# Kernel tuning notes

Hardware: AMD Instinct MI355X
Metric: run time of the kernel (lower is better)

Reference implementation:

```python
import jax, jax.numpy as jnp
import numpy as np

DIM = 768
HEADS = 12
HEAD_DIM = DIM // HEADS
B, S = 2, 2048
EPS = 1e-5


def _layernorm(x, w, b):
    mu = jnp.mean(x, axis=-1, keepdims=True)
    var = jnp.mean(jnp.square(x - mu), axis=-1, keepdims=True)
    return (x - mu) * jax.lax.rsqrt(var + EPS) * w + b


def setup_inputs() -> dict:
    key = jax.random.key(0)
    ks = jax.random.split(key, 16)
    sc = 1.0 / np.sqrt(DIM)
    inp = {
        'x': jax.random.normal(ks[0], (B, S, DIM), jnp.float32),
        'bias': jax.random.normal(ks[1], (HEADS, B, S, S), jnp.float32),
        'mask': jax.random.randint(ks[2], (1, B, S, S), 0, 2, jnp.int32),
        'ln1_w': jnp.ones((DIM,), jnp.float32),
        'ln1_b': jnp.zeros((DIM,), jnp.float32),
        'wq': jax.random.normal(ks[3], (DIM, DIM), jnp.float32) * sc,
        'bq': jnp.zeros((DIM,), jnp.float32),
        'wk': jax.random.normal(ks[4], (DIM, DIM), jnp.float32) * sc,
        'bk': jnp.zeros((DIM,), jnp.float32),
        'wv': jax.random.normal(ks[5], (DIM, DIM), jnp.float32) * sc,
        'bv': jnp.zeros((DIM,), jnp.float32),
        'wo': jax.random.normal(ks[6], (DIM, DIM), jnp.float32) * sc,
        'bo': jnp.zeros((DIM,), jnp.float32),
        'ln2_w': jnp.ones((DIM,), jnp.float32),
        'ln2_b': jnp.zeros((DIM,), jnp.float32),
        'w1': jax.random.normal(ks[7], (DIM, DIM), jnp.float32) * sc,
        'b1': jnp.zeros((DIM,), jnp.float32),
        'w2': jax.random.normal(ks[8], (DIM, DIM), jnp.float32) * sc,
        'b2': jnp.zeros((DIM,), jnp.float32),
    }
    return inp


def _split_heads(t):
    # [B,S,D] -> [H,B,S,Dh]  (matches torch view + permute(2,0,1,3))
    return t.reshape(B, S, HEADS, HEAD_DIM).transpose(2, 0, 1, 3)


def reference(x, bias, mask, ln1_w, ln1_b, wq, bq, wk, bk, wv, bv, wo, bo,
              ln2_w, ln2_b, w1, b1, w2, b2):
    xn = _layernorm(x, ln1_w, ln1_b)
    q = _split_heads(xn @ wq + bq)
    k = _split_heads(xn @ wk + bk)
    v = _split_heads(xn @ wv + bv)
    # scores: [H,B,Sq,Sk]; bias added BEFORE scaling, then masked, then scaled softmax
    scores = jnp.einsum('hbqd,hbkd->hbqk', q, k) + bias
    scores = jnp.where(mask == 0, jnp.float32(-1e20), scores)
    probs = jax.nn.softmax(scores / np.sqrt(HEAD_DIM), axis=-1)
    attn = jnp.einsum('hbqk,hbkd->hbqd', probs, v)
    attn = attn.transpose(1, 2, 0, 3).reshape(B, S, DIM)
    x = x + (attn @ wo + bo)
    xn = _layernorm(x, ln2_w, ln2_b)
    h = jax.nn.relu(xn @ w1 + b1)
    x = x + (h @ w2 + b2)
    return x
```

## Files before the change

### kernel.cpp

```cpp
#include <hip/hip_runtime.h>
#include <math.h>

#define DIMM 768
#define SEQ 2048
#define BATB 2
#define NHEAD 12
#define DHEAD 64
#define ROWS 4096

typedef __attribute__((ext_vector_type(8))) short bf16x8;
typedef __attribute__((ext_vector_type(4))) float f32x4;
typedef unsigned short ushort_t;
typedef unsigned int uint_t;

union U16 { int4 i; ushort_t u[8]; };

__device__ __forceinline__ ushort_t f2b(float f) {
    uint_t u = __float_as_uint(f);
    return (ushort_t)((u + 0x7FFFu + ((u >> 16) & 1u)) >> 16);
}

__device__ __forceinline__ void gl16(const ushort_t* g, ushort_t* l) {
    __builtin_amdgcn_global_load_lds(
        (const __attribute__((address_space(1))) unsigned int*)g,
        (__attribute__((address_space(3))) unsigned int*)l,
        16, 0, 0);
}

struct WPtrs { const float* s[6]; };
struct BPtrs { const float* p[3]; };

__global__ __launch_bounds__(256) void wtrans_k(WPtrs wp, ushort_t* __restrict__ dst)
{
    __shared__ float T[64][65];
    int wi = blockIdx.z;
    const float* in = wp.s[wi];
    ushort_t* out = dst + (size_t)wi * (DIMM * DIMM);
    int kb = blockIdx.y * 64, nb = blockIdx.x * 64;
    int t = threadIdx.x;
    int kl = t >> 4, nl = (t & 15) * 4;
    #pragma unroll
    for (int it = 0; it < 4; it++) {
        float4 a = *(const float4*)&in[(size_t)(kb + kl + it * 16) * DIMM + nb + nl];
        T[kl + it * 16][nl + 0] = a.x;
        T[kl + it * 16][nl + 1] = a.y;
        T[kl + it * 16][nl + 2] = a.z;
        T[kl + it * 16][nl + 3] = a.w;
    }
    __syncthreads();
    int no = t >> 2, ko = (t & 3) * 16;
    #pragma unroll
    for (int j = 0; j < 2; j++) {
        U16 u;
        #pragma unroll
        for (int c = 0; c < 8; c++) u.u[c] = f2b(T[ko + j * 8 + c][no]);
        *(int4*)&out[(size_t)(nb + no) * DIMM + kb + ko + j * 8] = u.i;
    }
}

__global__ __launch_bounds__(256) void ln_k(const float* __restrict__ x,
                                            const float* __restrict__ w,
                                            const float* __restrict__ b,
                                            ushort_t* __restrict__ out)
{
    int row = blockIdx.x;
    int tid = threadIdx.x;
    const float* xr = x + (size_t)row * DIMM;
    float v0 = xr[tid], v1 = xr[tid + 256], v2 = xr[tid + 512];
    float s  = v0 + v1 + v2;
    float ss = v0 * v0 + v1 * v1 + v2 * v2;
    #pragma unroll
    for (int off = 32; off > 0; off >>= 1) {
        s  += __shfl_down(s,  off);
        ss += __shfl_down(ss, off);
    }
    __shared__ float ws_[4], wss_[4];
    __shared__ float mu_s, rs_s;
    int lane = tid & 63, wid = tid >> 6;
    if (lane == 0) { ws_[wid] = s; wss_[wid] = ss; }
    __syncthreads();
    if (tid == 0) {
        float S1 = ws_[0] + ws_[1] + ws_[2] + ws_[3];
        float S2 = wss_[0] + wss_[1] + wss_[2] + wss_[3];
        float m = S1 * (1.0f / DIMM);
        float var = S2 * (1.0f / DIMM) - m * m;
        mu_s = m;
        rs_s = rsqrtf(var + 1e-5f);
    }
    __syncthreads();
    float mu = mu_s, rs = rs_s;
    ushort_t* orow = out + (size_t)row * DIMM;
    orow[tid]       = f2b((v0 - mu) * rs * w[tid]       + b[tid]);
    orow[tid + 256] = f2b((v1 - mu) * rs * w[tid + 256] + b[tid + 256]);
    orow[tid + 512] = f2b((v2 - mu) * rs * w[tid + 512] + b[tid + 512]);
}

template<int ASRC, int OMODE, bool RELU, bool RES, int NB>
__global__ __launch_bounds__(256) void mgemm_k(const ushort_t* __restrict__ A,
                                               const ushort_t* __restrict__ BT,
                                               BPtrs bias,
                                               const float* __restrict__ res,
                                               void* __restrict__ outv)
{
    __shared__ alignas(16) ushort_t Asl[8 * 64 * 8];
    __shared__ alignas(16) ushort_t Bsl[8 * 64 * 8];
    int tid = threadIdx.x;
    int lane = tid & 63, w = tid >> 6;
    int colBase = blockIdx.x * 64, rowBase = blockIdx.y * 64;

    size_t offA[2], offB[2];
    ushort_t* dstA[2];
    ushort_t* dstB[2];
    const size_t strideA = (ASRC == 1) ? (size_t)64 : (size_t)BATB * SEQ * DHEAD;
    #pragma unroll
    for (int i = 0; i < 2; i++) {
        int slot = i * 4 + w;
        {
            int sm = ((slot >> 1) << 4) | (lane & 15);
            int c  = ((slot & 1) << 2) | (lane >> 4);
            if (ASRC == 1) {
                offA[i] = (size_t)(rowBase + sm) * DIMM + 8 * c;
            } else {
                int r = rowBase + sm;
                offA[i] = ((size_t)(r >> 11) * SEQ + (r & 2047)) * DHEAD + 8 * c;
            }
            dstA[i] = &Asl[(size_t)(i * 256 + w * 64) * 8];
        }
        {
            int sm = ((slot & 3) << 4) | (lane & 15);
            int c  = ((slot >> 2) << 2) | (lane >> 4);
            offB[i] = (size_t)(colBase + sm) * DIMM + 8 * c;
            dstB[i] = &Bsl[(size_t)(i * 256 + w * 64) * 8];
        }
    }

    f32x4 acc[4];
    #pragma unroll
    for (int nt = 0; nt < 4; nt++) { f32x4 z = {0.f, 0.f, 0.f, 0.f}; acc[nt] = z; }

    for (int t = 0; t < DIMM / 64; t++) {
        gl16(A  + offA[0], dstA[0]);
        gl16(A  + offA[1], dstA[1]);
        gl16(BT + offB[0], dstB[0]);
        gl16(BT + offB[1], dstB[1]);
        offA[0] += strideA; offA[1] += strideA;
        offB[0] += 64;      offB[1] += 64;
        __syncthreads();
        bf16x8 a0 = *(bf16x8*)&Asl[((w * 2 + 0) * 64 + lane) * 8];
        bf16x8 a1 = *(bf16x8*)&Asl[((w * 2 + 1) * 64 + lane) * 8];
        #pragma unroll
        for (int nt = 0; nt < 4; nt++) {
            bf16x8 b0 = *(bf16x8*)&Bsl[((0 * 4 + nt) * 64 + lane) * 8];
            bf16x8 b1 = *(bf16x8*)&Bsl[((1 * 4 + nt) * 64 + lane) * 8];
            acc[nt] = __builtin_amdgcn_mfma_f32_16x16x32_bf16(a0, b0, acc[nt], 0, 0, 0);
            acc[nt] = __builtin_amdgcn_mfma_f32_16x16x32_bf16(a1, b1, acc[nt], 0, 0, 0);
        }
        __syncthreads();
    }
    int wi = (NB == 3) ? (int)(blockIdx.x / 12) : 0;
    const float* bp_ = bias.p[wi];
    int nLoc0 = colBase - wi * DIMM;
    int col_l = lane & 15, quad = lane >> 4;
    #pragma unroll
    for (int nt = 0; nt < 4; nt++) {
        int n = colBase + nt * 16 + col_l;
        float bn = bp_[nLoc0 + nt * 16 + col_l];
        #pragma unroll
        for (int r = 0; r < 4; r++) {
            int row = rowBase + w * 16 + quad * 4 + r;
            float v = acc[nt][r] + bn;
            if (RELU) v = fmaxf(v, 0.0f);
            if (RES)  v += res[(size_t)row * DIMM + n];
            if (OMODE == 0) {
                ((float*)outv)[(size_t)row * DIMM + n] = v;
            } else if (OMODE == 1) {
                ((ushort_t*)outv)[(size_t)row * DIMM + n] = f2b(v);
            } else {
                ((ushort_t*)outv)[((size_t)((n >> 6) * BATB + (row >> 11)) * SEQ + (row & 2047)) * DHEAD + (n & 63)] = f2b(v);
            }
        }
    }
}

__global__ __launch_bounds__(256) void attn_k(const ushort_t* __restrict__ q,
                                              const ushort_t* __restrict__ k,
                                              const ushort_t* __restrict__ v,
                                              const float* __restrict__ bias,
                                              const int* __restrict__ mask,
                                              ushort_t* __restrict__ out)
{
    __shared__ alignas(16) ushort_t Kf[8 * 64 * 8];
    __shared__ alignas(16) ushort_t Vf[8 * 64 * 8];
    __shared__ alignas(16) ushort_t Pf[8 * 64 * 8];
    int tid = threadIdx.x, lane = tid & 63, w = tid >> 6;
    int col_l = lane & 15, quad = lane >> 4;
    int qbase = blockIdx.x * 64;
    int hb = blockIdx.y;
    const ushort_t* qp = q + (size_t)hb * SEQ * DHEAD;
    const ushort_t* kp = k + (size_t)hb * SEQ * DHEAD;
    const ushort_t* vp = v + (size_t)hb * SEQ * DHEAD;
    const float* bp = bias + (size_t)hb * SEQ * SEQ;
    const int*   mp = mask + (size_t)(hb & 1) * SEQ * SEQ;

    bf16x8 qF0 = *(const bf16x8*)&qp[(size_t)(qbase + w * 16 + col_l) * DHEAD + (quad * 8)];
    bf16x8 qF1 = *(const bf16x8*)&qp[(size_t)(qbase + w * 16 + col_l) * DHEAD + 32 + (quad * 8)];

    size_t offK[2];
    ushort_t* dstK[2];
    #pragma unroll
    for (int i = 0; i < 2; i++) {
        int slot = i * 4 + w;
        int sn = ((slot & 3) << 4) | (lane & 15);
        int c  = ((slot >> 2) << 2) | (lane >> 4);
        offK[i] = (size_t)sn * DHEAD + 8 * c;
        dstK[i] = &Kf[(size_t)(i * 256 + w * 64) * 8];
    }

    f32x4 O[4];
    #pragma unroll
    for (int nt = 0; nt < 4; nt++) { f32x4 z = {0.f, 0.f, 0.f, 0.f}; O[nt] = z; }
    float m_run[4], l_run[4];
    #pragma unroll
    for (int r = 0; r < 4; r++) { m_run[r] = -1e30f; l_run[r] = 0.0f; }

    int j0 = (tid >> 3) * 2, e0 = (tid & 7) * 8;
    const float C2 = 0.18033688011112042f;

    for (int kvb = 0; kvb < SEQ; kvb += 64) {
        gl16(kp + (size_t)kvb * DHEAD + offK[0], dstK[0]);
        gl16(kp + (size_t)kvb * DHEAD + offK[1], dstK[1]);
        {
            U16 g0, g1;
            g0.i = *(const int4*)&vp[(size_t)(kvb + j0) * DHEAD + e0];
            g1.i = *(const int4*)&vp[(size_t)(kvb + j0 + 1) * DHEAD + e0];
            int js = j0 >> 5, grp = (j0 & 31) >> 3, i0 = j0 & 7;
            #pragma unroll
            for (int c = 0; c < 8; c++) {
                int n = e0 + c;
                uint_t pk = (uint_t)g0.u[c] | ((uint_t)g1.u[c] << 16);
                int idx = ((js * 4 + (n >> 4)) * 64 + ((n & 15) | (grp << 4))) * 8 + i0;
                *(uint_t*)&Vf[idx] = pk;
            }
        }
        float bl[4][4]; int ml[4][4];
        #pragma unroll
        for (int nt = 0; nt < 4; nt++) {
            int col = kvb + nt * 16 + col_l;
            #pragma unroll
            for (int r = 0; r < 4; r++) {
                int qrow = qbase + w * 16 + quad * 4 + r;
                bl[nt][r] = bp[(size_t)qrow * SEQ + col];
                ml[nt][r] = mp[(size_t)qrow * SEQ + col];
            }
        }
        __syncthreads();
        f32x4 S[4];
        #pragma unroll
        for (int nt = 0; nt < 4; nt++) {
            bf16x8 b0 = *(bf16x8*)&Kf[((0 * 4 + nt) * 64 + lane) * 8];
            bf16x8 b1 = *(bf16x8*)&Kf[((1 * 4 + nt) * 64 + lane) * 8];
            f32x4 z = {0.f, 0.f, 0.f, 0.f};
            z = __builtin_amdgcn_mfma_f32_16x16x32_bf16(qF0, b0, z, 0, 0, 0);
            S[nt] = __builtin_amdgcn_mfma_f32_16x16x32_bf16(qF1, b1, z, 0, 0, 0);
        }
        float lg[4][4];
        #pragma unroll
        for (int nt = 0; nt < 4; nt++)
            #pragma unroll
            for (int r = 0; r < 4; r++)
                lg[nt][r] = ml[nt][r] ? (S[nt][r] + bl[nt][r]) * C2 : -2.0e18f;
        #pragma unroll
        for (int r = 0; r < 4; r++) {
            float mx = fmaxf(fmaxf(lg[0][r], lg[1][r]), fmaxf(lg[2][r], lg[3][r]));
            mx = fmaxf(mx, __shfl_xor(mx, 1));
            mx = fmaxf(mx, __shfl_xor(mx, 2));
            mx = fmaxf(mx, __shfl_xor(mx, 4));
            mx = fmaxf(mx, __shfl_xor(mx, 8));
            if (!__all(mx - m_run[r] <= 4.0f)) {
                float mnew = fmaxf(m_run[r], mx);
                float alpha = __builtin_amdgcn_exp2f(m_run[r] - mnew);
                m_run[r] = mnew;
                l_run[r] *= alpha;
                #pragma unroll
                for (int nt = 0; nt < 4; nt++) O[nt][r] *= alpha;
            }
            float mcur = m_run[r];
            float rs = 0.0f;
            #pragma unroll
            for (int nt = 0; nt < 4; nt++) {
                float p = __builtin_amdgcn_exp2f(lg[nt][r] - mcur);
                lg[nt][r] = p;
                rs += p;
            }
            rs += __shfl_xor(rs, 1);
            rs += __shfl_xor(rs, 2);
            rs += __shfl_xor(rs, 4);
            rs += __shfl_xor(rs, 8);
            l_run[r] += rs;
        }
        #pragma unroll
        for (int nt = 0; nt < 4; nt++) {
            int j = nt * 16 + col_l;
            #pragma unroll
            for (int r = 0; r < 4; r++) {
                ushort_t pu = f2b(lg[nt][r]);
                uint_t po = (uint_t)(unsigned)__shfl_xor((int)pu, 1);
                if ((lane & 1) == 0) {
                    int m = quad * 4 + r;
                    int idx = ((w * 2 + (j >> 5)) * 64 + (m | (((j & 31) >> 3) << 4))) * 8 + (j & 7);
                    *(uint_t*)&Pf[idx] = (uint_t)pu | (po << 16);
                }
            }
        }
        #pragma unroll
        for (int js = 0; js < 2; js++) {
            bf16x8 pF = *(bf16x8*)&Pf[((w * 2 + js) * 64 + lane) * 8];
            #pragma unroll
            for (int nt = 0; nt < 4; nt++) {
                bf16x8 vF = *(bf16x8*)&Vf[((js * 4 + nt) * 64 + lane) * 8];
                O[nt] = __builtin_amdgcn_mfma_f32_16x16x32_bf16(pF, vF, O[nt], 0, 0, 0);
            }
        }
        __syncthreads();
    }
    float inv[4];
    #pragma unroll
    for (int r = 0; r < 4; r++) inv[r] = 1.0f / l_run[r];
    #pragma unroll
    for (int nt = 0; nt < 4; nt++)
        #pragma unroll
        for (int r = 0; r < 4; r++) {
            int row = qbase + w * 16 + quad * 4 + r;
            out[((size_t)hb * SEQ + row) * DHEAD + nt * 16 + col_l] = f2b(O[nt][r] * inv[r]);
        }
}

extern "C" void kernel_launch(void* const* d_in, const int* in_sizes, int n_in,
                              void* d_out, int out_size, void* d_ws, size_t ws_size,
                              hipStream_t stream)
{
    const float* x    = (const float*)d_in[0];
    const float* bias = (const float*)d_in[1];
    const int*   mask = (const int*)d_in[2];
    const float* ln1w = (const float*)d_in[3];
    const float* ln1b = (const float*)d_in[4];
    const float* wq   = (const float*)d_in[5];
    const float* bq   = (const float*)d_in[6];
    const float* wk   = (const float*)d_in[7];
    const float* bk   = (const float*)d_in[8];
    const float* wv   = (const float*)d_in[9];
    const float* bv   = (const float*)d_in[10];
    const float* wo   = (const float*)d_in[11];
    const float* bo   = (const float*)d_in[12];
    const float* ln2w = (const float*)d_in[13];
    const float* ln2b = (const float*)d_in[14];
    const float* w1   = (const float*)d_in[15];
    const float* b1   = (const float*)d_in[16];
    const float* w2   = (const float*)d_in[17];
    const float* b2   = (const float*)d_in[18];

    const size_t WSZ = (size_t)DIMM * DIMM;
    const size_t ABUF = (size_t)ROWS * DIMM;

    ushort_t* wsu  = (ushort_t*)d_ws;
    ushort_t* wT   = wsu;
    ushort_t* qb   = wsu + 6 * WSZ;
    ushort_t* kbuf = qb + ABUF;
    ushort_t* vbuf = kbuf + ABUF;
    ushort_t* xn1  = vbuf + ABUF;
    float*    x1   = (float*)(xn1 + ABUF);
    ushort_t* hid  = qb;

    WPtrs wp; wp.s[0] = wq; wp.s[1] = wk; wp.s[2] = wv; wp.s[3] = wo; wp.s[4] = w1; wp.s[5] = w2;
    BPtrs bqkv; bqkv.p[0] = bq; bqkv.p[1] = bk; bqkv.p[2] = bv;
    BPtrs bbo;  bbo.p[0]  = bo; bbo.p[1]  = bo; bbo.p[2]  = bo;
    BPtrs bb1;  bb1.p[0]  = b1; bb1.p[1]  = b1; bb1.p[2]  = b1;
    BPtrs bb2;  bb2.p[0]  = b2; bb2.p[1]  = b2; bb2.p[2]  = b2;

    dim3 gg(12, 64), gb(256);
    wtrans_k<<<dim3(12, 12, 6), 256, 0, stream>>>(wp, wT);
    ln_k<<<ROWS, 256, 0, stream>>>(x, ln1w, ln1b, xn1);
    mgemm_k<1, 2, false, false, 3><<<dim3(36, 64), gb, 0, stream>>>(xn1, wT, bqkv, nullptr, qb);
    attn_k<<<dim3(32, 24), 256, 0, stream>>>(qb, kbuf, vbuf, bias, mask, xn1);
    mgemm_k<2, 0, false, true, 1><<<gg, gb, 0, stream>>>(xn1, wT + 3 * WSZ, bbo, x, x1);
    ln_k<<<ROWS, 256, 0, stream>>>(x1, ln2w, ln2b, xn1);
    mgemm_k<1, 1, true, false, 1><<<gg, gb, 0, stream>>>(xn1, wT + 4 * WSZ, bb1, nullptr, hid);
    mgemm_k<1, 0, false, true, 1><<<gg, gb, 0, stream>>>(hid, wT + 5 * WSZ, bb2, x1, (float*)d_out);
}
```

Measured before the change: 783.0 us.

## Double-buffer LDS tiles in GEMM and attention kernels with register prefetch

```diff
diff --git a/kernel.cpp b/kernel.cpp
--- a/kernel.cpp
+++ b/kernel.cpp
@@ -102,15 +102,14 @@
                                                const float* __restrict__ res,
                                                void* __restrict__ outv)
 {
-    __shared__ alignas(16) ushort_t Asl[8 * 64 * 8];
-    __shared__ alignas(16) ushort_t Bsl[8 * 64 * 8];
+    __shared__ alignas(16) ushort_t Asl[2][8 * 64 * 8];
+    __shared__ alignas(16) ushort_t Bsl[2][8 * 64 * 8];
     int tid = threadIdx.x;
     int lane = tid & 63, w = tid >> 6;
     int colBase = blockIdx.x * 64, rowBase = blockIdx.y * 64;
 
     size_t offA[2], offB[2];
-    ushort_t* dstA[2];
-    ushort_t* dstB[2];
+    int lbA[2], lbB[2];
     const size_t strideA = (ASRC == 1) ? (size_t)64 : (size_t)BATB * SEQ * DHEAD;
     #pragma unroll
     for (int i = 0; i < 2; i++) {
@@ -124,13 +123,13 @@
                 int r = rowBase + sm;
                 offA[i] = ((size_t)(r >> 11) * SEQ + (r & 2047)) * DHEAD + 8 * c;
             }
-            dstA[i] = &Asl[(size_t)(i * 256 + w * 64) * 8];
+            lbA[i] = (i * 256 + w * 64) * 8;
         }
         {
             int sm = ((slot & 3) << 4) | (lane & 15);
             int c  = ((slot >> 2) << 2) | (lane >> 4);
             offB[i] = (size_t)(colBase + sm) * DIMM + 8 * c;
-            dstB[i] = &Bsl[(size_t)(i * 256 + w * 64) * 8];
+            lbB[i] = (i * 256 + w * 64) * 8;
         }
     }
 
@@ -138,24 +137,51 @@
     #pragma unroll
     for (int nt = 0; nt < 4; nt++) { f32x4 z = {0.f, 0.f, 0.f, 0.f}; acc[nt] = z; }
 
-    for (int t = 0; t < DIMM / 64; t++) {
-        gl16(A  + offA[0], dstA[0]);
-        gl16(A  + offA[1], dstA[1]);
-        gl16(BT + offB[0], dstB[0]);
-        gl16(BT + offB[1], dstB[1]);
+    const int NT = DIMM / 64;
+
+    gl16(A  + offA[0], &Asl[0][lbA[0]]);
+    gl16(A  + offA[1], &Asl[0][lbA[1]]);
+    gl16(BT + offB[0], &Bsl[0][lbB[0]]);
+    gl16(BT + offB[1], &Bsl[0][lbB[1]]);
+    offA[0] += strideA; offA[1] += strideA;
+    offB[0] += 64;      offB[1] += 64;
+
+    int p = 0;
+    for (int t = 0; t < NT - 1; ++t) {
+        gl16(A  + offA[0], &Asl[p ^ 1][lbA[0]]);
+        gl16(A  + offA[1], &Asl[p ^ 1][lbA[1]]);
+        gl16(BT + offB[0], &Bsl[p ^ 1][lbB[0]]);
+        gl16(BT + offB[1], &Bsl[p ^ 1][lbB[1]]);
         offA[0] += strideA; offA[1] += strideA;
         offB[0] += 64;      offB[1] += 64;
-        __syncthreads();
-        bf16x8 a0 = *(bf16x8*)&Asl[((w * 2 + 0) * 64 + lane) * 8];
-        bf16x8 a1 = *(bf16x8*)&Asl[((w * 2 + 1) * 64 + lane) * 8];
+        asm volatile("s_waitcnt vmcnt(4)" ::: "memory");
+        __builtin_amdgcn_sched_barrier(0);
+        __builtin_amdgcn_s_barrier();
+        bf16x8 a0 = *(bf16x8*)&Asl[p][((w * 2 + 0) * 64 + lane) * 8];
+        bf16x8 a1 = *(bf16x8*)&Asl[p][((w * 2 + 1) * 64 + lane) * 8];
         #pragma unroll
         for (int nt = 0; nt < 4; nt++) {
-            bf16x8 b0 = *(bf16x8*)&Bsl[((0 * 4 + nt) * 64 + lane) * 8];
-            bf16x8 b1 = *(bf16x8*)&Bsl[((1 * 4 + nt) * 64 + lane) * 8];
+            bf16x8 b0 = *(bf16x8*)&Bsl[p][((0 * 4 + nt) * 64 + lane) * 8];
+            bf16x8 b1 = *(bf16x8*)&Bsl[p][((1 * 4 + nt) * 64 + lane) * 8];
             acc[nt] = __builtin_amdgcn_mfma_f32_16x16x32_bf16(a0, b0, acc[nt], 0, 0, 0);
             acc[nt] = __builtin_amdgcn_mfma_f32_16x16x32_bf16(a1, b1, acc[nt], 0, 0, 0);
         }
-        __syncthreads();
+        __builtin_amdgcn_s_barrier();
+        p ^= 1;
+    }
+    asm volatile("s_waitcnt vmcnt(0)" ::: "memory");
+    __builtin_amdgcn_sched_barrier(0);
+    __builtin_amdgcn_s_barrier();
+    {
+        bf16x8 a0 = *(bf16x8*)&Asl[p][((w * 2 + 0) * 64 + lane) * 8];
+        bf16x8 a1 = *(bf16x8*)&Asl[p][((w * 2 + 1) * 64 + lane) * 8];
+        #pragma unroll
+        for (int nt = 0; nt < 4; nt++) {
+            bf16x8 b0 = *(bf16x8*)&Bsl[p][((0 * 4 + nt) * 64 + lane) * 8];
+            bf16x8 b1 = *(bf16x8*)&Bsl[p][((1 * 4 + nt) * 64 + lane) * 8];
+            acc[nt] = __builtin_amdgcn_mfma_f32_16x16x32_bf16(a0, b0, acc[nt], 0, 0, 0);
+            acc[nt] = __builtin_amdgcn_mfma_f32_16x16x32_bf16(a1, b1, acc[nt], 0, 0, 0);
+        }
     }
     int wi = (NB == 3) ? (int)(blockIdx.x / 12) : 0;
     const float* bp_ = bias.p[wi];
@@ -189,8 +215,8 @@
                                               const int* __restrict__ mask,
                                               ushort_t* __restrict__ out)
 {
-    __shared__ alignas(16) ushort_t Kf[8 * 64 * 8];
-    __shared__ alignas(16) ushort_t Vf[8 * 64 * 8];
+    __shared__ alignas(16) ushort_t Kf[2][8 * 64 * 8];
+    __shared__ alignas(16) ushort_t Vf[2][8 * 64 * 8];
     __shared__ alignas(16) ushort_t Pf[8 * 64 * 8];
     int tid = threadIdx.x, lane = tid & 63, w = tid >> 6;
     int col_l = lane & 15, quad = lane >> 4;
@@ -205,16 +231,19 @@
     bf16x8 qF0 = *(const bf16x8*)&qp[(size_t)(qbase + w * 16 + col_l) * DHEAD + (quad * 8)];
     bf16x8 qF1 = *(const bf16x8*)&qp[(size_t)(qbase + w * 16 + col_l) * DHEAD + 32 + (quad * 8)];
 
-    size_t offK[2];
-    ushort_t* dstK[2];
-    #pragma unroll
-    for (int i = 0; i < 2; i++) {
-        int slot = i * 4 + w;
-        int sn = ((slot & 3) << 4) | (lane & 15);
-        int c  = ((slot >> 2) << 2) | (lane >> 4);
-        offK[i] = (size_t)sn * DHEAD + 8 * c;
-        dstK[i] = &Kf[(size_t)(i * 256 + w * 64) * 8];
-    }
+    int sn = tid >> 2, sko = (tid & 3) * 16;
+    int kidx[2];
+    #pragma unroll
+    for (int jj = 0; jj < 2; jj++) {
+        int kk = sko + jj * 8;
+        int slot = (kk >> 5) * 4 + (sn >> 4);
+        int ln = (sn & 15) | (((kk & 31) >> 3) << 4);
+        kidx[jj] = (slot * 64 + ln) * 8;
+    }
+    size_t koff = (size_t)sn * DHEAD + sko;
+    int j0 = (tid >> 3) * 2, e0 = (tid & 7) * 8;
+    int js = j0 >> 5, grp = (j0 & 31) >> 3, i0 = j0 & 7;
+    size_t voff = (size_t)j0 * DHEAD + e0;
 
     f32x4 O[4];
     #pragma unroll
@@ -223,25 +252,35 @@
     #pragma unroll
     for (int r = 0; r < 4; r++) { m_run[r] = -1e30f; l_run[r] = 0.0f; }
 
-    int j0 = (tid >> 3) * 2, e0 = (tid & 7) * 8;
     const float C2 = 0.18033688011112042f;
 
+    int4 kr0 = *(const int4*)&kp[koff];
+    int4 kr1 = *(const int4*)&kp[koff + 8];
+    int4 vr0 = *(const int4*)&vp[voff];
+    int4 vr1 = *(const int4*)&vp[voff + DHEAD];
+    *(int4*)&Kf[0][kidx[0]] = kr0;
+    *(int4*)&Kf[0][kidx[1]] = kr1;
+    {
+        U16 g0, g1; g0.i = vr0; g1.i = vr1;
+        #pragma unroll
+        for (int c = 0; c < 8; c++) {
+            int n = e0 + c;
+            uint_t pk = (uint_t)g0.u[c] | ((uint_t)g1.u[c] << 16);
+            int idx = ((js * 4 + (n >> 4)) * 64 + ((n & 15) | (grp << 4))) * 8 + i0;
+            *(uint_t*)&Vf[0][idx] = pk;
+        }
+    }
+    {
+        size_t b1 = (size_t)64 * DHEAD;
+        kr0 = *(const int4*)&kp[b1 + koff];
+        kr1 = *(const int4*)&kp[b1 + koff + 8];
+        vr0 = *(const int4*)&vp[b1 + voff];
+        vr1 = *(const int4*)&vp[b1 + voff + DHEAD];
+    }
+    __syncthreads();
+
+    int p = 0;
     for (int kvb = 0; kvb < SEQ; kvb += 64) {
-        gl16(kp + (size_t)kvb * DHEAD + offK[0], dstK[0]);
-        gl16(kp + (size_t)kvb * DHEAD + offK[1], dstK[1]);
-        {
-            U16 g0, g1;
-            g0.i = *(const int4*)&vp[(size_t)(kvb + j0) * DHEAD + e0];
-            g1.i = *(const int4*)&vp[(size_t)(kvb + j0 + 1) * DHEAD + e0];
-            int js = j0 >> 5, grp = (j0 & 31) >> 3, i0 = j0 & 7;
-            #pragma unroll
-            for (int c = 0; c < 8; c++) {
-                int n = e0 + c;
-                uint_t pk = (uint_t)g0.u[c] | ((uint_t)g1.u[c] << 16);
-                int idx = ((js * 4 + (n >> 4)) * 64 + ((n & 15) | (grp << 4))) * 8 + i0;
-                *(uint_t*)&Vf[idx] = pk;
-            }
-        }
         float bl[4][4]; int ml[4][4];
         #pragma unroll
         for (int nt = 0; nt < 4; nt++) {
@@ -253,16 +292,17 @@
                 ml[nt][r] = mp[(size_t)qrow * SEQ + col];
             }
         }
-        __syncthreads();
         f32x4 S[4];
+        __builtin_amdgcn_s_setprio(1);
         #pragma unroll
         for (int nt = 0; nt < 4; nt++) {
-            bf16x8 b0 = *(bf16x8*)&Kf[((0 * 4 + nt) * 64 + lane) * 8];
-            bf16x8 b1 = *(bf16x8*)&Kf[((1 * 4 + nt) * 64 + lane) * 8];
+            bf16x8 b0 = *(bf16x8*)&Kf[p][((0 * 4 + nt) * 64 + lane) * 8];
+            bf16x8 b1 = *(bf16x8*)&Kf[p][((1 * 4 + nt) * 64 + lane) * 8];
             f32x4 z = {0.f, 0.f, 0.f, 0.f};
             z = __builtin_amdgcn_mfma_f32_16x16x32_bf16(qF0, b0, z, 0, 0, 0);
             S[nt] = __builtin_amdgcn_mfma_f32_16x16x32_bf16(qF1, b1, z, 0, 0, 0);
         }
+        __builtin_amdgcn_s_setprio(0);
         float lg[4][4];
         #pragma unroll
         for (int nt = 0; nt < 4; nt++)
@@ -288,15 +328,36 @@
             float rs = 0.0f;
             #pragma unroll
             for (int nt = 0; nt < 4; nt++) {
-                float p = __builtin_amdgcn_exp2f(lg[nt][r] - mcur);
-                lg[nt][r] = p;
-                rs += p;
+                float pp = __builtin_amdgcn_exp2f(lg[nt][r] - mcur);
+                lg[nt][r] = pp;
+                rs += pp;
             }
             rs += __shfl_xor(rs, 1);
             rs += __shfl_xor(rs, 2);
             rs += __shfl_xor(rs, 4);
             rs += __shfl_xor(rs, 8);
             l_run[r] += rs;
+        }
+        if (kvb + 64 < SEQ) {
+            *(int4*)&Kf[p ^ 1][kidx[0]] = kr0;
+            *(int4*)&Kf[p ^ 1][kidx[1]] = kr1;
+            {
+                U16 g0, g1; g0.i = vr0; g1.i = vr1;
+                #pragma unroll
+                for (int c = 0; c < 8; c++) {
+                    int n = e0 + c;
+                    uint_t pk = (uint_t)g0.u[c] | ((uint_t)g1.u[c] << 16);
+                    int idx = ((js * 4 + (n >> 4)) * 64 + ((n & 15) | (grp << 4))) * 8 + i0;
+                    *(uint_t*)&Vf[p ^ 1][idx] = pk;
+                }
+            }
+            if (kvb + 128 < SEQ) {
+                size_t b2 = (size_t)(kvb + 128) * DHEAD;
+                kr0 = *(const int4*)&kp[b2 + koff];
+                kr1 = *(const int4*)&kp[b2 + koff + 8];
+                vr0 = *(const int4*)&vp[b2 + voff];
+                vr1 = *(const int4*)&vp[b2 + voff + DHEAD];
+            }
         }
         #pragma unroll
         for (int nt = 0; nt < 4; nt++) {
@@ -312,16 +373,19 @@
                 }
             }
         }
-        #pragma unroll
-        for (int js = 0; js < 2; js++) {
-            bf16x8 pF = *(bf16x8*)&Pf[((w * 2 + js) * 64 + lane) * 8];
+        __builtin_amdgcn_s_setprio(1);
+        #pragma unroll
+        for (int jss = 0; jss < 2; jss++) {
+            bf16x8 pF = *(bf16x8*)&Pf[((w * 2 + jss) * 64 + lane) * 8];
             #pragma unroll
             for (int nt = 0; nt < 4; nt++) {
-                bf16x8 vF = *(bf16x8*)&Vf[((js * 4 + nt) * 64 + lane) * 8];
+                bf16x8 vF = *(bf16x8*)&Vf[p][((jss * 4 + nt) * 64 + lane) * 8];
                 O[nt] = __builtin_amdgcn_mfma_f32_16x16x32_bf16(pF, vF, O[nt], 0, 0, 0);
             }
         }
+        __builtin_amdgcn_s_setprio(0);
         __syncthreads();
+        p ^= 1;
     }
     float inv[4];
     #pragma unroll
```

Measured after the change: 835.2 us. 6.7% more time.

## Double-buffer K/V tiles and prefetch bias/mask in attention loop

Applied to the files above, without the earlier changes.

```diff
diff --git a/kernel.cpp b/kernel.cpp
--- a/kernel.cpp
+++ b/kernel.cpp
@@ -182,15 +182,15 @@
     }
 }
 
-__global__ __launch_bounds__(256) void attn_k(const ushort_t* __restrict__ q,
-                                              const ushort_t* __restrict__ k,
-                                              const ushort_t* __restrict__ v,
-                                              const float* __restrict__ bias,
-                                              const int* __restrict__ mask,
-                                              ushort_t* __restrict__ out)
+__global__ __launch_bounds__(256, 4) void attn_k(const ushort_t* __restrict__ q,
+                                                 const ushort_t* __restrict__ k,
+                                                 const ushort_t* __restrict__ v,
+                                                 const float* __restrict__ bias,
+                                                 const int* __restrict__ mask,
+                                                 ushort_t* __restrict__ out)
 {
-    __shared__ alignas(16) ushort_t Kf[8 * 64 * 8];
-    __shared__ alignas(16) ushort_t Vf[8 * 64 * 8];
+    __shared__ alignas(16) ushort_t Kf[2][8 * 64 * 8];
+    __shared__ alignas(16) ushort_t Vf[2][8 * 64 * 8];
     __shared__ alignas(16) ushort_t Pf[8 * 64 * 8];
     int tid = threadIdx.x, lane = tid & 63, w = tid >> 6;
     int col_l = lane & 15, quad = lane >> 4;
@@ -205,16 +205,18 @@
     bf16x8 qF0 = *(const bf16x8*)&qp[(size_t)(qbase + w * 16 + col_l) * DHEAD + (quad * 8)];
     bf16x8 qF1 = *(const bf16x8*)&qp[(size_t)(qbase + w * 16 + col_l) * DHEAD + 32 + (quad * 8)];
 
-    size_t offK[2];
-    ushort_t* dstK[2];
+    size_t offK[2]; int lbK[2];
     #pragma unroll
     for (int i = 0; i < 2; i++) {
         int slot = i * 4 + w;
         int sn = ((slot & 3) << 4) | (lane & 15);
         int c  = ((slot >> 2) << 2) | (lane >> 4);
         offK[i] = (size_t)sn * DHEAD + 8 * c;
-        dstK[i] = &Kf[(size_t)(i * 256 + w * 64) * 8];
-    }
+        lbK[i] = (i * 256 + w * 64) * 8;
+    }
+    int j0 = (tid >> 3) * 2, e0 = (tid & 7) * 8;
+    int js = j0 >> 5, grp = (j0 & 31) >> 3, i0 = j0 & 7;
+    size_t voff = (size_t)j0 * DHEAD + e0;
 
     f32x4 O[4];
     #pragma unroll
@@ -223,52 +225,88 @@
     #pragma unroll
     for (int r = 0; r < 4; r++) { m_run[r] = -1e30f; l_run[r] = 0.0f; }
 
-    int j0 = (tid >> 3) * 2, e0 = (tid & 7) * 8;
     const float C2 = 0.18033688011112042f;
 
+    gl16(kp + offK[0], &Kf[0][lbK[0]]);
+    gl16(kp + offK[1], &Kf[0][lbK[1]]);
+    int4 vr0 = *(const int4*)&vp[voff];
+    int4 vr1 = *(const int4*)&vp[voff + DHEAD];
+    float blN[4][4]; int mlN[4][4];
+    #pragma unroll
+    for (int nt = 0; nt < 4; nt++) {
+        int col = nt * 16 + col_l;
+        #pragma unroll
+        for (int r = 0; r < 4; r++) {
+            int qrow = qbase + w * 16 + quad * 4 + r;
+            blN[nt][r] = bp[(size_t)qrow * SEQ + col];
+            mlN[nt][r] = mp[(size_t)qrow * SEQ + col];
+        }
+    }
+    {
+        U16 g0, g1; g0.i = vr0; g1.i = vr1;
+        #pragma unroll
+        for (int c = 0; c < 8; c++) {
+            int n = e0 + c;
+            uint_t pk = (uint_t)g0.u[c] | ((uint_t)g1.u[c] << 16);
+            int idx = ((js * 4 + (n >> 4)) * 64 + ((n & 15) | (grp << 4))) * 8 + i0;
+            *(uint_t*)&Vf[0][idx] = pk;
+        }
+    }
+    {
+        size_t b1 = (size_t)64 * DHEAD;
+        vr0 = *(const int4*)&vp[b1 + voff];
+        vr1 = *(const int4*)&vp[b1 + voff + DHEAD];
+    }
+    __syncthreads();
+
+    int p = 0;
     for (int kvb = 0; kvb < SEQ; kvb += 64) {
-        gl16(kp + (size_t)kvb * DHEAD + offK[0], dstK[0]);
-        gl16(kp + (size_t)kvb * DHEAD + offK[1], dstK[1]);
-        {
-            U16 g0, g1;
-            g0.i = *(const int4*)&vp[(size_t)(kvb + j0) * DHEAD + e0];
-            g1.i = *(const int4*)&vp[(size_t)(kvb + j0 + 1) * DHEAD + e0];
-            int js = j0 >> 5, grp = (j0 & 31) >> 3, i0 = j0 & 7;
-            #pragma unroll
-            for (int c = 0; c < 8; c++) {
-                int n = e0 + c;
-                uint_t pk = (uint_t)g0.u[c] | ((uint_t)g1.u[c] << 16);
-                int idx = ((js * 4 + (n >> 4)) * 64 + ((n & 15) | (grp << 4))) * 8 + i0;
-                *(uint_t*)&Vf[idx] = pk;
-            }
-        }
-        float bl[4][4]; int ml[4][4];
+        f32x4 S[4];
+        __builtin_amdgcn_s_setprio(1);
         #pragma unroll
         for (int nt = 0; nt < 4; nt++) {
-            int col = kvb + nt * 16 + col_l;
-            #pragma unroll
-            for (int r = 0; r < 4; r++) {
-                int qrow = qbase + w * 16 + quad * 4 + r;
-                bl[nt][r] = bp[(size_t)qrow * SEQ + col];
-                ml[nt][r] = mp[(size_t)qrow * SEQ + col];
-            }
-        }
-        __syncthreads();
-        f32x4 S[4];
-        #pragma unroll
-        for (int nt = 0; nt < 4; nt++) {
-            bf16x8 b0 = *(bf16x8*)&Kf[((0 * 4 + nt) * 64 + lane) * 8];
-            bf16x8 b1 = *(bf16x8*)&Kf[((1 * 4 + nt) * 64 + lane) * 8];
+            bf16x8 b0 = *(bf16x8*)&Kf[p][((0 * 4 + nt) * 64 + lane) * 8];
+            bf16x8 b1 = *(bf16x8*)&Kf[p][((1 * 4 + nt) * 64 + lane) * 8];
             f32x4 z = {0.f, 0.f, 0.f, 0.f};
             z = __builtin_amdgcn_mfma_f32_16x16x32_bf16(qF0, b0, z, 0, 0, 0);
             S[nt] = __builtin_amdgcn_mfma_f32_16x16x32_bf16(qF1, b1, z, 0, 0, 0);
         }
+        __builtin_amdgcn_s_setprio(0);
         float lg[4][4];
         #pragma unroll
         for (int nt = 0; nt < 4; nt++)
             #pragma unroll
             for (int r = 0; r < 4; r++)
-                lg[nt][r] = ml[nt][r] ? (S[nt][r] + bl[nt][r]) * C2 : -2.0e18f;
+                lg[nt][r] = mlN[nt][r] ? (S[nt][r] + blN[nt][r]) * C2 : -2.0e18f;
+        if (kvb + 64 < SEQ) {
+            #pragma unroll
+            for (int nt = 0; nt < 4; nt++) {
+                int col = kvb + 64 + nt * 16 + col_l;
+                #pragma unroll
+                for (int r = 0; r < 4; r++) {
+                    int qrow = qbase + w * 16 + quad * 4 + r;
+                    blN[nt][r] = bp[(size_t)qrow * SEQ + col];
+                    mlN[nt][r] = mp[(size_t)qrow * SEQ + col];
+                }
+            }
+            gl16(kp + (size_t)(kvb + 64) * DHEAD + offK[0], &Kf[p ^ 1][lbK[0]]);
+            gl16(kp + (size_t)(kvb + 64) * DHEAD + offK[1], &Kf[p ^ 1][lbK[1]]);
+            {
+                U16 g0, g1; g0.i = vr0; g1.i = vr1;
+                #pragma unroll
+                for (int c = 0; c < 8; c++) {
+                    int n = e0 + c;
+                    uint_t pk = (uint_t)g0.u[c] | ((uint_t)g1.u[c] << 16);
+                    int idx = ((js * 4 + (n >> 4)) * 64 + ((n & 15) | (grp << 4))) * 8 + i0;
+                    *(uint_t*)&Vf[p ^ 1][idx] = pk;
+                }
+            }
+            if (kvb + 128 < SEQ) {
+                size_t b2 = (size_t)(kvb + 128) * DHEAD;
+                vr0 = *(const int4*)&vp[b2 + voff];
+                vr1 = *(const int4*)&vp[b2 + voff + DHEAD];
+            }
+        }
         #pragma unroll
         for (int r = 0; r < 4; r++) {
             float mx = fmaxf(fmaxf(lg[0][r], lg[1][r]), fmaxf(lg[2][r], lg[3][r]));
@@ -288,9 +326,9 @@
             float rs = 0.0f;
             #pragma unroll
             for (int nt = 0; nt < 4; nt++) {
-                float p = __builtin_amdgcn_exp2f(lg[nt][r] - mcur);
-                lg[nt][r] = p;
-                rs += p;
+                float pp = __builtin_amdgcn_exp2f(lg[nt][r] - mcur);
+                lg[nt][r] = pp;
+                rs += pp;
             }
             rs += __shfl_xor(rs, 1);
             rs += __shfl_xor(rs, 2);
@@ -312,16 +350,19 @@
                 }
             }
         }
-        #pragma unroll
-        for (int js = 0; js < 2; js++) {
-            bf16x8 pF = *(bf16x8*)&Pf[((w * 2 + js) * 64 + lane) * 8];
+        __builtin_amdgcn_s_setprio(1);
+        #pragma unroll
+        for (int jss = 0; jss < 2; jss++) {
+            bf16x8 pF = *(bf16x8*)&Pf[((w * 2 + jss) * 64 + lane) * 8];
             #pragma unroll
             for (int nt = 0; nt < 4; nt++) {
-                bf16x8 vF = *(bf16x8*)&Vf[((js * 4 + nt) * 64 + lane) * 8];
+                bf16x8 vF = *(bf16x8*)&Vf[p][((jss * 4 + nt) * 64 + lane) * 8];
                 O[nt] = __builtin_amdgcn_mfma_f32_16x16x32_bf16(pF, vF, O[nt], 0, 0, 0);
             }
         }
+        __builtin_amdgcn_s_setprio(0);
         __syncthreads();
+        p ^= 1;
     }
     float inv[4];
     #pragma unroll
```

Measured after the change: 1.381 ms. 1.76x slower.

## Enlarge GEMM block tile to 128x128 with 2x2 warp layout and register reuse

Applied to the files above, without the earlier changes.

```diff
diff --git a/kernel.cpp b/kernel.cpp
--- a/kernel.cpp
+++ b/kernel.cpp
@@ -102,81 +102,86 @@
                                                const float* __restrict__ res,
                                                void* __restrict__ outv)
 {
-    __shared__ alignas(16) ushort_t Asl[8 * 64 * 8];
-    __shared__ alignas(16) ushort_t Bsl[8 * 64 * 8];
+    __shared__ alignas(16) ushort_t Asl[16 * 64 * 8];
+    __shared__ alignas(16) ushort_t Bsl[16 * 64 * 8];
     int tid = threadIdx.x;
     int lane = tid & 63, w = tid >> 6;
-    int colBase = blockIdx.x * 64, rowBase = blockIdx.y * 64;
-
-    size_t offA[2], offB[2];
-    ushort_t* dstA[2];
-    ushort_t* dstB[2];
+    int wr = w >> 1, wc = w & 1;
+    int colBase = blockIdx.x * 128, rowBase = blockIdx.y * 128;
+
+    size_t offA[4], offB[4];
+    ushort_t* dstA[4];
+    ushort_t* dstB[4];
     const size_t strideA = (ASRC == 1) ? (size_t)64 : (size_t)BATB * SEQ * DHEAD;
     #pragma unroll
-    for (int i = 0; i < 2; i++) {
-        int slot = i * 4 + w;
-        {
-            int sm = ((slot >> 1) << 4) | (lane & 15);
-            int c  = ((slot & 1) << 2) | (lane >> 4);
-            if (ASRC == 1) {
-                offA[i] = (size_t)(rowBase + sm) * DIMM + 8 * c;
-            } else {
-                int r = rowBase + sm;
-                offA[i] = ((size_t)(r >> 11) * SEQ + (r & 2047)) * DHEAD + 8 * c;
-            }
-            dstA[i] = &Asl[(size_t)(i * 256 + w * 64) * 8];
-        }
-        {
-            int sm = ((slot & 3) << 4) | (lane & 15);
-            int c  = ((slot >> 2) << 2) | (lane >> 4);
-            offB[i] = (size_t)(colBase + sm) * DIMM + 8 * c;
-            dstB[i] = &Bsl[(size_t)(i * 256 + w * 64) * 8];
-        }
-    }
-
-    f32x4 acc[4];
-    #pragma unroll
-    for (int nt = 0; nt < 4; nt++) { f32x4 z = {0.f, 0.f, 0.f, 0.f}; acc[nt] = z; }
+    for (int i = 0; i < 4; i++) {
+        int s  = i * 4 + w;
+        int mt = s >> 1, ks = s & 1;
+        int rr = mt * 16 + (lane & 15);
+        int kk = ks * 32 + (lane >> 4) * 8;
+        if (ASRC == 1) {
+            offA[i] = (size_t)(rowBase + rr) * DIMM + kk;
+        } else {
+            int r = rowBase + rr;
+            offA[i] = ((size_t)(r >> 11) * SEQ + (r & 2047)) * DHEAD + kk;
+        }
+        dstA[i] = &Asl[(size_t)s * 64 * 8];
+        offB[i] = (size_t)(colBase + rr) * DIMM + kk;
+        dstB[i] = &Bsl[(size_t)s * 64 * 8];
+    }
+
+    f32x4 acc[4][4];
+    #pragma unroll
+    for (int mi = 0; mi < 4; mi++)
+        #pragma unroll
+        for (int ni = 0; ni < 4; ni++) { f32x4 z = {0.f, 0.f, 0.f, 0.f}; acc[mi][ni] = z; }
 
     for (int t = 0; t < DIMM / 64; t++) {
-        gl16(A  + offA[0], dstA[0]);
-        gl16(A  + offA[1], dstA[1]);
-        gl16(BT + offB[0], dstB[0]);
-        gl16(BT + offB[1], dstB[1]);
-        offA[0] += strideA; offA[1] += strideA;
-        offB[0] += 64;      offB[1] += 64;
+        #pragma unroll
+        for (int i = 0; i < 4; i++) { gl16(A  + offA[i], dstA[i]); offA[i] += strideA; }
+        #pragma unroll
+        for (int i = 0; i < 4; i++) { gl16(BT + offB[i], dstB[i]); offB[i] += 64; }
         __syncthreads();
-        bf16x8 a0 = *(bf16x8*)&Asl[((w * 2 + 0) * 64 + lane) * 8];
-        bf16x8 a1 = *(bf16x8*)&Asl[((w * 2 + 1) * 64 + lane) * 8];
-        #pragma unroll
-        for (int nt = 0; nt < 4; nt++) {
-            bf16x8 b0 = *(bf16x8*)&Bsl[((0 * 4 + nt) * 64 + lane) * 8];
-            bf16x8 b1 = *(bf16x8*)&Bsl[((1 * 4 + nt) * 64 + lane) * 8];
-            acc[nt] = __builtin_amdgcn_mfma_f32_16x16x32_bf16(a0, b0, acc[nt], 0, 0, 0);
-            acc[nt] = __builtin_amdgcn_mfma_f32_16x16x32_bf16(a1, b1, acc[nt], 0, 0, 0);
+        bf16x8 b[4][2];
+        #pragma unroll
+        for (int ni = 0; ni < 4; ni++)
+            #pragma unroll
+            for (int ks = 0; ks < 2; ks++)
+                b[ni][ks] = *(bf16x8*)&Bsl[((((wc * 4 + ni) * 2 + ks)) * 64 + lane) * 8];
+        #pragma unroll
+        for (int mi = 0; mi < 4; mi++) {
+            bf16x8 a0 = *(bf16x8*)&Asl[((((wr * 4 + mi) * 2 + 0)) * 64 + lane) * 8];
+            bf16x8 a1 = *(bf16x8*)&Asl[((((wr * 4 + mi) * 2 + 1)) * 64 + lane) * 8];
+            #pragma unroll
+            for (int ni = 0; ni < 4; ni++) {
+                acc[mi][ni] = __builtin_amdgcn_mfma_f32_16x16x32_bf16(a0, b[ni][0], acc[mi][ni], 0, 0, 0);
+                acc[mi][ni] = __builtin_amdgcn_mfma_f32_16x16x32_bf16(a1, b[ni][1], acc[mi][ni], 0, 0, 0);
+            }
         }
         __syncthreads();
     }
-    int wi = (NB == 3) ? (int)(blockIdx.x / 12) : 0;
+    int wi = (NB == 3) ? (colBase / DIMM) : 0;
     const float* bp_ = bias.p[wi];
-    int nLoc0 = colBase - wi * DIMM;
     int col_l = lane & 15, quad = lane >> 4;
     #pragma unroll
-    for (int nt = 0; nt < 4; nt++) {
-        int n = colBase + nt * 16 + col_l;
-        float bn = bp_[nLoc0 + nt * 16 + col_l];
-        #pragma unroll
-        for (int r = 0; r < 4; r++) {
-            int row = rowBase + w * 16 + quad * 4 + r;
-            float v = acc[nt][r] + bn;
-            if (RELU) v = fmaxf(v, 0.0f);
-            if (RES)  v += res[(size_t)row * DIMM + n];
-            if (OMODE == 0) {
-                ((float*)outv)[(size_t)row * DIMM + n] = v;
-            } else if (OMODE == 1) {
-                ((ushort_t*)outv)[(size_t)row * DIMM + n] = f2b(v);
-            } else {
-                ((ushort_t*)outv)[((size_t)((n >> 6) * BATB + (row >> 11)) * SEQ + (row & 2047)) * DHEAD + (n & 63)] = f2b(v);
+    for (int ni = 0; ni < 4; ni++) {
+        int n = colBase + wc * 64 + ni * 16 + col_l;
+        float bn = bp_[n - wi * DIMM];
+        #pragma unroll
+        for (int mi = 0; mi < 4; mi++) {
+            #pragma unroll
+            for (int r = 0; r < 4; r++) {
+                int row = rowBase + wr * 64 + mi * 16 + quad * 4 + r;
+                float v = acc[mi][ni][r] + bn;
+                if (RELU) v = fmaxf(v, 0.0f);
+                if (RES)  v += res[(size_t)row * DIMM + n];
+                if (OMODE == 0) {
+                    ((float*)outv)[(size_t)row * DIMM + n] = v;
+                } else if (OMODE == 1) {
+                    ((ushort_t*)outv)[(size_t)row * DIMM + n] = f2b(v);
+                } else {
+                    ((ushort_t*)outv)[((size_t)((n >> 6) * BATB + (row >> 11)) * SEQ + (row & 2047)) * DHEAD + (n & 63)] = f2b(v);
+                }
             }
         }
     }
@@ -288,9 +293,9 @@
             float rs = 0.0f;
             #pragma unroll
             for (int nt = 0; nt < 4; nt++) {
-                float p = __builtin_amdgcn_exp2f(lg[nt][r] - mcur);
-                lg[nt][r] = p;
-                rs += p;
+                float pp = __builtin_amdgcn_exp2f(lg[nt][r] - mcur);
+                lg[nt][r] = pp;
+                rs += pp;
             }
             rs += __shfl_xor(rs, 1);
             rs += __shfl_xor(rs, 2);
@@ -313,11 +318,11 @@
             }
         }
         #pragma unroll
-        for (int js = 0; js < 2; js++) {
-            bf16x8 pF = *(bf16x8*)&Pf[((w * 2 + js) * 64 + lane) * 8];
+        for (int jss = 0; jss < 2; jss++) {
+            bf16x8 pF = *(bf16x8*)&Pf[((w * 2 + jss) * 64 + lane) * 8];
             #pragma unroll
             for (int nt = 0; nt < 4; nt++) {
-                bf16x8 vF = *(bf16x8*)&Vf[((js * 4 + nt) * 64 + lane) * 8];
+                bf16x8 vF = *(bf16x8*)&Vf[((jss * 4 + nt) * 64 + lane) * 8];
                 O[nt] = __builtin_amdgcn_mfma_f32_16x16x32_bf16(pF, vF, O[nt], 0, 0, 0);
             }
         }
@@ -377,10 +382,10 @@
     BPtrs bb1;  bb1.p[0]  = b1; bb1.p[1]  = b1; bb1.p[2]  = b1;
     BPtrs bb2;  bb2.p[0]  = b2; bb2.p[1]  = b2; bb2.p[2]  = b2;
 
-    dim3 gg(12, 64), gb(256);
+    dim3 gg(6, 32), gb(256);
     wtrans_k<<<dim3(12, 12, 6), 256, 0, stream>>>(wp, wT);
     ln_k<<<ROWS, 256, 0, stream>>>(x, ln1w, ln1b, xn1);
-    mgemm_k<1, 2, false, false, 3><<<dim3(36, 64), gb, 0, stream>>>(xn1, wT, bqkv, nullptr, qb);
+    mgemm_k<1, 2, false, false, 3><<<dim3(18, 32), gb, 0, stream>>>(xn1, wT, bqkv, nullptr, qb);
     attn_k<<<dim3(32, 24), 256, 0, stream>>>(qb, kbuf, vbuf, bias, mask, xn1);
     mgemm_k<2, 0, false, true, 1><<<gg, gb, 0, stream>>>(xn1, wT + 3 * WSZ, bbo, x, x1);
     ln_k<<<ROWS, 256, 0, stream>>>(x1, ln2w, ln2b, xn1);
```

Result: slower. 798.9 us (+2.0%).
